# Performance work log

Measured on AMD Instinct MI355X. Metric: run time of the kernel, lower is better.

## Reference

```python
import jax, jax.numpy as jnp
import numpy as np

EPS = 1e-5

def _ln(x, g, b):
    m = jnp.mean(x, axis=-1, keepdims=True)
    v = jnp.mean(jnp.square(x - m), axis=-1, keepdims=True)
    return (x - m) * jax.lax.rsqrt(v + EPS) * g + b

def setup_inputs() -> dict:
    key = jax.random.key(0)
    ks = jax.random.split(key, 20)
    B, F = 262144, 768
    sizes = [F, 512, 256, 128, 1]  # LN(d_in) -> Linear(d_in, d_out) per block
    inp = {"input": jax.random.normal(ks[0], (B, F), dtype=jnp.float32)}
    for i in range(4):
        din, dout = sizes[i], sizes[i + 1]
        inp[f"g{i}"] = jnp.ones((din,), dtype=jnp.float32)
        inp[f"b{i}"] = jnp.zeros((din,), dtype=jnp.float32)
        bound = 1.0 / np.sqrt(din)
        inp[f"W{i}"] = jax.random.uniform(ks[1 + 2 * i], (dout, din), dtype=jnp.float32, minval=-bound, maxval=bound)
        inp[f"c{i}"] = jax.random.uniform(ks[2 + 2 * i], (dout,), dtype=jnp.float32, minval=-bound, maxval=bound)
    return inp

def reference(input, g0, b0, W0, c0, g1, b1, W1, c1, g2, b2, W2, c2, g3, b3, W3, c3):
    x = input
    params = [(g0, b0, W0, c0), (g1, b1, W1, c1), (g2, b2, W2, c2), (g3, b3, W3, c3)]
    for i, (g, b, W, c) in enumerate(params):
        x = _ln(x, g, b)
        x = x @ W.T + c
        if i != 3:
            x = jax.nn.elu(x)
    return jnp.squeeze(x, axis=-1)  # [B]
```

## Files before the change

kernel.cpp:

```cpp
#include <hip/hip_runtime.h>
#include <hip/hip_fp16.h>
#include <math.h>

typedef _Float16 half_t;
typedef half_t half2_t __attribute__((ext_vector_type(2)));
typedef half_t half4_t __attribute__((ext_vector_type(4)));
typedef half_t half8_t __attribute__((ext_vector_type(8)));
typedef float f32x4 __attribute__((ext_vector_type(4)));

#define LN_EPS 1e-5f
#define FDOT2(a, b, c) __builtin_amdgcn_fdot2((a), (b), (c), false)

__global__ void pack_weights(const float* __restrict__ W0, const float* __restrict__ g0,
                             const float* __restrict__ W1, const float* __restrict__ g1,
                             const float* __restrict__ W2, const float* __restrict__ g2,
                             half_t* __restrict__ ws) {
    int sid = blockIdx.x * 256 + threadIdx.x;
    const float* W; const float* g; int K, T, off;
    if (sid < 49152)      { W = W0; g = g0; K = 768; T = 24; off = 0; }
    else if (sid < 65536) { W = W1; g = g1; K = 512; T = 16; off = 49152; sid -= 49152; }
    else if (sid < 69632) { W = W2; g = g2; K = 256; T = 8;  off = 65536; sid -= 65536; }
    else return;
    const int l   = sid & 63;
    const int t   = (sid >> 6) % T;
    const int cbg = (sid >> 6) / T;
    const int n   = (l & 15) + 16 * cbg;
    const int k0  = 32 * t + 8 * (l >> 4);
    const float* src = W + (size_t)n * K + k0;
    const float* gs  = g + k0;
    half8_t v;
    #pragma unroll
    for (int jq = 0; jq < 8; jq++) v[jq] = (half_t)(src[jq] * gs[jq]);
    *(half8_t*)(ws + (size_t)(off + sid) * 8) = v;
}

__global__ void fold_bias(const float* __restrict__ W0, const float* __restrict__ g0,
                          const float* __restrict__ b0, const float* __restrict__ c0,
                          const float* __restrict__ W1, const float* __restrict__ g1,
                          const float* __restrict__ b1, const float* __restrict__ c1,
                          const float* __restrict__ W2, const float* __restrict__ g2,
                          const float* __restrict__ b2, const float* __restrict__ c2,
                          const float* __restrict__ W3, const float* __restrict__ g3,
                          const float* __restrict__ b3, const float* __restrict__ c3,
                          float* __restrict__ f) {
    const int gw   = (blockIdx.x * 256 + threadIdx.x) >> 6;
    const int lane = threadIdx.x & 63;
    if (gw == 896) {
        float s = 0.f, cb_ = 0.f;
        for (int k = lane; k < 128; k += 64) {
            const float wg = W3[k] * g3[k];
            f[1792 + k] = wg;
            s += wg; cb_ += W3[k] * b3[k];
        }
        #pragma unroll
        for (int m = 1; m < 64; m <<= 1) { s += __shfl_xor(s, m); cb_ += __shfl_xor(cb_, m); }
        if (lane == 0) { f[1920] = s; f[1921] = cb_ + c3[0]; }
        return;
    }
    const float *W, *g, *b, *cc; int K, n; float *sf, *cf;
    if (gw < 512)      { W = W0; g = g0; b = b0; cc = c0; K = 768; n = gw;       sf = f;        cf = f + 512; }
    else if (gw < 768) { W = W1; g = g1; b = b1; cc = c1; K = 512; n = gw - 512; sf = f + 1024; cf = f + 1280; }
    else if (gw < 896) { W = W2; g = g2; b = b2; cc = c2; K = 256; n = gw - 768; sf = f + 1536; cf = f + 1664; }
    else return;
    const float* Wr = W + (size_t)n * K;
    float s = 0.f, cb_ = 0.f;
    for (int k = lane; k < K; k += 64) { const float wg = Wr[k] * g[k]; s += wg; cb_ += Wr[k] * b[k]; }
    #pragma unroll
    for (int m = 1; m < 64; m <<= 1) { s += __shfl_xor(s, m); cb_ += __shfl_xor(cb_, m); }
    if (lane == 0) { sf[n] = s; cf[n] = cb_ + cc[n]; }
}

__global__ __launch_bounds__(512, 4)
void fused_mlp(const float* __restrict__ x_in,
               const half_t* __restrict__ W0p, const half_t* __restrict__ W1p,
               const half_t* __restrict__ W2p, const float* __restrict__ f,
               float* __restrict__ out)
{
    __shared__ half_t frag[32768];
    __shared__ float row_m[64], row_rs[64];
    __shared__ float ps[2][64], pq[2][64];
    __shared__ half2_t w3h[64];

    const int tid  = threadIdx.x;
    const int lane = tid & 63;
    const int wv   = tid >> 6;
    const int grp  = lane >> 4;
    const int cl   = lane & 15;
    const int row  = tid >> 3;
    const int jj   = tid & 7;
    const int rbw  = row >> 4;
    const long r0  = (long)blockIdx.x * 64;
    const float* xrow = x_in + (r0 + row) * 768;

    const int rb_s = wv & 3;
    const int th_s = wv >> 2;

    const float* s0f = f;        const float* c0f = f + 512;
    const float* s1f = f + 1024; const float* c1f = f + 1280;
    const float* s2f = f + 1536; const float* c2f = f + 1664;

    const half2_t one2 = {(half_t)1.f, (half_t)1.f};

    if (tid < 64) {
        half2_t w; w[0] = (half_t)f[1792 + 2 * tid]; w[1] = (half_t)f[1793 + 2 * tid];
        w3h[tid] = w;
    }

    float s = 0.f, ss = 0.f;
    f32x4 vb[4];

    auto stage_load = [&](int c) {
        const float* xp = xrow + 128 * c + 4 * jj;
        #pragma unroll
        for (int i = 0; i < 4; i++)
            vb[i] = __builtin_nontemporal_load((const f32x4*)(xp + 32 * i));
    };
    auto stage_write = [&](int c) {
        half_t* fb = frag + 8192 * (c & 1);
        const int hg = jj >> 1, jo = 4 * (jj & 1);
        #pragma unroll
        for (int i = 0; i < 4; i++) {
            const f32x4 v = vb[i];
            half2_t h01; h01[0] = (half_t)v[0]; h01[1] = (half_t)v[1];
            half2_t h23; h23[0] = (half_t)v[2]; h23[1] = (half_t)v[3];
            s  = FDOT2(h01, one2, s);  s  = FDOT2(h23, one2, s);
            ss = FDOT2(h01, h01, ss);  ss = FDOT2(h23, h23, ss);
            half4_t hv; hv[0] = h01[0]; hv[1] = h01[1]; hv[2] = h23[0]; hv[3] = h23[1];
            *(half4_t*)(&fb[((i * 4 + rbw) * 64 + ((row & 15) + 16 * hg)) * 8 + jo]) = hv;
        }
    };

    f32x4 acc0[4][4];
    #pragma unroll
    for (int rb = 0; rb < 4; rb++)
        #pragma unroll
        for (int cb = 0; cb < 4; cb++) acc0[rb][cb] = 0.f;

    auto gemm0 = [&](int c) {
        const half_t* fb = frag + 8192 * (c & 1);
        const half_t* wp = W0p + (size_t)(4 * wv * 24 + 4 * c) * 512 + lane * 8;
        half8_t bA[4], bB[4];
        #pragma unroll
        for (int cb = 0; cb < 4; cb++) bA[cb] = *(const half8_t*)(wp + cb * 12288);
        #pragma unroll
        for (int tt = 0; tt < 4; tt++) {
            half8_t* cur = (tt & 1) ? bB : bA;
            half8_t* nxt = (tt & 1) ? bA : bB;
            if (tt < 3) {
                #pragma unroll
                for (int cb = 0; cb < 4; cb++)
                    nxt[cb] = *(const half8_t*)(wp + (tt + 1) * 512 + cb * 12288);
            }
            half8_t af[4];
            #pragma unroll
            for (int rb = 0; rb < 4; rb++)
                af[rb] = *(const half8_t*)(&fb[((tt * 4 + rb) * 64 + lane) * 8]);
            #pragma unroll
            for (int cb = 0; cb < 4; cb++)
                #pragma unroll
                for (int rb = 0; rb < 4; rb++)
                    acc0[rb][cb] = __builtin_amdgcn_mfma_f32_16x16x32_f16(af[rb], cur[cb], acc0[rb][cb], 0, 0, 0);
        }
    };

    stage_load(0); stage_write(0);
    __syncthreads();
    #pragma unroll 1
    for (int c = 0; c < 6; c++) {
        if (c < 5) stage_load(c + 1);
        gemm0(c);
        if (c < 5) stage_write(c + 1);
        if (c == 4) {
            s  += __shfl_xor(s, 1);  s  += __shfl_xor(s, 2);  s  += __shfl_xor(s, 4);
            ss += __shfl_xor(ss, 1); ss += __shfl_xor(ss, 2); ss += __shfl_xor(ss, 4);
            if (jj == 0) {
                const float mm = s * (1.f / 768.f);
                row_m[row]  = mm;
                row_rs[row] = 1.f / sqrtf(ss * (1.f / 768.f) - mm * mm + LN_EPS);
            }
        }
        __syncthreads();
    }

    {
        float sv[4], cv[4];
        #pragma unroll
        for (int cb = 0; cb < 4; cb++) {
            const int c = cl + 16 * (4 * wv + cb);
            sv[cb] = s0f[c]; cv[cb] = c0f[c];
        }
        #pragma unroll
        for (int rb = 0; rb < 4; rb++)
            #pragma unroll
            for (int v = 0; v < 4; v++) {
                const int r = 16 * rb + 4 * grp + v;
                const float rm = row_m[r], rr = row_rs[r];
                #pragma unroll
                for (int cb = 0; cb < 4; cb++) {
                    float y = rr * (acc0[rb][cb][v] - rm * sv[cb]) + cv[cb];
                    acc0[rb][cb][v] = y > 0.f ? y : (__expf(y) - 1.f);
                }
            }
        #pragma unroll
        for (int cb = 0; cb < 4; cb++) {
            const int c = cl + 16 * (4 * wv + cb);
            const int t = c >> 5, j = c & 7, sc = 16 * ((c >> 3) & 3);
            #pragma unroll
            for (int rb = 0; rb < 4; rb++)
                #pragma unroll
                for (int v = 0; v < 4; v++)
                    frag[((t * 4 + rb) * 64 + (4 * grp + v + sc)) * 8 + j] = (half_t)acc0[rb][cb][v];
        }
    }
    __syncthreads();

    {
        float s_ = 0.f, q_ = 0.f;
        #pragma unroll
        for (int i = 0; i < 8; i++) {
            const int t = 8 * th_s + i;
            const half8_t h = *(const half8_t*)(&frag[((t * 4 + rb_s) * 64 + lane) * 8]);
            half2_t p0 = {h[0], h[1]}, p1 = {h[2], h[3]}, p2 = {h[4], h[5]}, p3 = {h[6], h[7]};
            s_ = FDOT2(p0, one2, s_); s_ = FDOT2(p1, one2, s_);
            s_ = FDOT2(p2, one2, s_); s_ = FDOT2(p3, one2, s_);
            q_ = FDOT2(p0, p0, q_);   q_ = FDOT2(p1, p1, q_);
            q_ = FDOT2(p2, p2, q_);   q_ = FDOT2(p3, p3, q_);
        }
        s_ += __shfl_xor(s_, 16); s_ += __shfl_xor(s_, 32);
        q_ += __shfl_xor(q_, 16); q_ += __shfl_xor(q_, 32);
        if (lane < 16) { ps[th_s][16 * rb_s + lane] = s_; pq[th_s][16 * rb_s + lane] = q_; }
    }
    __syncthreads();
    if (tid < 64) {
        const float a_ = ps[0][tid] + ps[1][tid];
        const float b_ = pq[0][tid] + pq[1][tid];
        const float mm = a_ * (1.f / 512.f);
        row_m[tid]  = mm;
        row_rs[tid] = 1.f / sqrtf(b_ * (1.f / 512.f) - mm * mm + LN_EPS);
    }

    f32x4 acc1[4][2];
    #pragma unroll
    for (int rb = 0; rb < 4; rb++) { acc1[rb][0] = 0.f; acc1[rb][1] = 0.f; }
    {
        const half_t* wp = W1p + (size_t)(2 * wv * 16) * 512 + lane * 8;
        half8_t bA[2], bB[2];
        bA[0] = *(const half8_t*)(wp);
        bA[1] = *(const half8_t*)(wp + 8192);
        #pragma unroll
        for (int t = 0; t < 16; t++) {
            half8_t* cur = (t & 1) ? bB : bA;
            half8_t* nxt = (t & 1) ? bA : bB;
            if (t < 15) {
                nxt[0] = *(const half8_t*)(wp + (t + 1) * 512);
                nxt[1] = *(const half8_t*)(wp + (t + 1) * 512 + 8192);
            }
            half8_t af[4];
            #pragma unroll
            for (int rb = 0; rb < 4; rb++)
                af[rb] = *(const half8_t*)(&frag[((t * 4 + rb) * 64 + lane) * 8]);
            #pragma unroll
            for (int cb = 0; cb < 2; cb++)
                #pragma unroll
                for (int rb = 0; rb < 4; rb++)
                    acc1[rb][cb] = __builtin_amdgcn_mfma_f32_16x16x32_f16(af[rb], cur[cb], acc1[rb][cb], 0, 0, 0);
        }
    }
    __syncthreads();

    {
        float sv[2], cv[2];
        #pragma unroll
        for (int cb = 0; cb < 2; cb++) {
            const int c = cl + 16 * (2 * wv + cb);
            sv[cb] = s1f[c]; cv[cb] = c1f[c];
        }
        #pragma unroll
        for (int rb = 0; rb < 4; rb++)
            #pragma unroll
            for (int v = 0; v < 4; v++) {
                const int r = 16 * rb + 4 * grp + v;
                const float rm = row_m[r], rr = row_rs[r];
                #pragma unroll
                for (int cb = 0; cb < 2; cb++) {
                    float y = rr * (acc1[rb][cb][v] - rm * sv[cb]) + cv[cb];
                    acc1[rb][cb][v] = y > 0.f ? y : (__expf(y) - 1.f);
                }
            }
        #pragma unroll
        for (int cb = 0; cb < 2; cb++) {
            const int c = cl + 16 * (2 * wv + cb);
            const int t = c >> 5, j = c & 7, sc = 16 * ((c >> 3) & 3);
            #pragma unroll
            for (int rb = 0; rb < 4; rb++)
                #pragma unroll
                for (int v = 0; v < 4; v++)
                    frag[((t * 4 + rb) * 64 + (4 * grp + v + sc)) * 8 + j] = (half_t)acc1[rb][cb][v];
        }
    }
    __syncthreads();

    {
        float s_ = 0.f, q_ = 0.f;
        #pragma unroll
        for (int i = 0; i < 4; i++) {
            const int t = 4 * th_s + i;
            const half8_t h = *(const half8_t*)(&frag[((t * 4 + rb_s) * 64 + lane) * 8]);
            half2_t p0 = {h[0], h[1]}, p1 = {h[2], h[3]}, p2 = {h[4], h[5]}, p3 = {h[6], h[7]};
            s_ = FDOT2(p0, one2, s_); s_ = FDOT2(p1, one2, s_);
            s_ = FDOT2(p2, one2, s_); s_ = FDOT2(p3, one2, s_);
            q_ = FDOT2(p0, p0, q_);   q_ = FDOT2(p1, p1, q_);
            q_ = FDOT2(p2, p2, q_);   q_ = FDOT2(p3, p3, q_);
        }
        s_ += __shfl_xor(s_, 16); s_ += __shfl_xor(s_, 32);
        q_ += __shfl_xor(q_, 16); q_ += __shfl_xor(q_, 32);
        if (lane < 16) { ps[th_s][16 * rb_s + lane] = s_; pq[th_s][16 * rb_s + lane] = q_; }
    }
    __syncthreads();
    if (tid < 64) {
        const float a_ = ps[0][tid] + ps[1][tid];
        const float b_ = pq[0][tid] + pq[1][tid];
        const float mm = a_ * (1.f / 256.f);
        row_m[tid]  = mm;
        row_rs[tid] = 1.f / sqrtf(b_ * (1.f / 256.f) - mm * mm + LN_EPS);
    }

    f32x4 acc2[4];
    #pragma unroll
    for (int rb = 0; rb < 4; rb++) acc2[rb] = 0.f;
    {
        const half_t* wp = W2p + (size_t)(wv * 8) * 512 + lane * 8;
        half8_t bA = *(const half8_t*)(wp);
        #pragma unroll
        for (int t = 0; t < 8; t++) {
            const half8_t cur = bA;
            if (t < 7) bA = *(const half8_t*)(wp + (t + 1) * 512);
            half8_t af[4];
            #pragma unroll
            for (int rb = 0; rb < 4; rb++)
                af[rb] = *(const half8_t*)(&frag[((t * 4 + rb) * 64 + lane) * 8]);
            #pragma unroll
            for (int rb = 0; rb < 4; rb++)
                acc2[rb] = __builtin_amdgcn_mfma_f32_16x16x32_f16(af[rb], cur, acc2[rb], 0, 0, 0);
        }
    }
    __syncthreads();

    {
        const int c2i = cl + 16 * wv;
        const float sv = s2f[c2i], cv = c2f[c2i];
        #pragma unroll
        for (int rb = 0; rb < 4; rb++)
            #pragma unroll
            for (int v = 0; v < 4; v++) {
                const int r = 16 * rb + 4 * grp + v;
                const float rm = row_m[r], rr = row_rs[r];
                float y = rr * (acc2[rb][v] - rm * sv) + cv;
                y = y > 0.f ? y : (__expf(y) - 1.f);
                frag[r * 136 + c2i] = (half_t)y;
            }
    }
    __syncthreads();

    {
        float s_ = 0.f, q_ = 0.f, d_ = 0.f;
        #pragma unroll
        for (int u = 0; u < 2; u++) {
            const int cb = jj * 16 + 8 * u;
            const int wi = cb >> 1;
            const half8_t h = *(const half8_t*)(frag + row * 136 + cb);
            half2_t p0 = {h[0], h[1]}, p1 = {h[2], h[3]}, p2 = {h[4], h[5]}, p3 = {h[6], h[7]};
            s_ = FDOT2(p0, one2, s_); s_ = FDOT2(p1, one2, s_);
            s_ = FDOT2(p2, one2, s_); s_ = FDOT2(p3, one2, s_);
            q_ = FDOT2(p0, p0, q_);   q_ = FDOT2(p1, p1, q_);
            q_ = FDOT2(p2, p2, q_);   q_ = FDOT2(p3, p3, q_);
            d_ = FDOT2(p0, w3h[wi], d_);     d_ = FDOT2(p1, w3h[wi + 1], d_);
            d_ = FDOT2(p2, w3h[wi + 2], d_); d_ = FDOT2(p3, w3h[wi + 3], d_);
        }
        s_ += __shfl_xor(s_, 1); s_ += __shfl_xor(s_, 2); s_ += __shfl_xor(s_, 4);
        q_ += __shfl_xor(q_, 1); q_ += __shfl_xor(q_, 2); q_ += __shfl_xor(q_, 4);
        d_ += __shfl_xor(d_, 1); d_ += __shfl_xor(d_, 2); d_ += __shfl_xor(d_, 4);
        if (jj == 0) {
            const float mm = s_ * (1.f / 128.f);
            const float rs = 1.f / sqrtf(q_ * (1.f / 128.f) - mm * mm + LN_EPS);
            out[r0 + row] = rs * (d_ - mm * f[1920]) + f[1921];
        }
    }
}

extern "C" void kernel_launch(void* const* d_in, const int* in_sizes, int n_in,
                              void* d_out, int out_size, void* d_ws, size_t ws_size,
                              hipStream_t stream) {
    const float* x  = (const float*)d_in[0];
    const float* g0 = (const float*)d_in[1];
    const float* b0 = (const float*)d_in[2];
    const float* W0 = (const float*)d_in[3];
    const float* c0 = (const float*)d_in[4];
    const float* g1 = (const float*)d_in[5];
    const float* b1 = (const float*)d_in[6];
    const float* W1 = (const float*)d_in[7];
    const float* c1 = (const float*)d_in[8];
    const float* g2 = (const float*)d_in[9];
    const float* b2 = (const float*)d_in[10];
    const float* W2 = (const float*)d_in[11];
    const float* c2 = (const float*)d_in[12];
    const float* g3 = (const float*)d_in[13];
    const float* b3 = (const float*)d_in[14];
    const float* W3 = (const float*)d_in[15];
    const float* c3 = (const float*)d_in[16];

    half_t* ws = (half_t*)d_ws;
    float*  f  = (float*)(ws + 557056);

    pack_weights<<<272, 256, 0, stream>>>(W0, g0, W1, g1, W2, g2, ws);
    fold_bias<<<225, 256, 0, stream>>>(W0, g0, b0, c0, W1, g1, b1, c1,
                                       W2, g2, b2, c2, W3, g3, b3, c3, f);

    const int nrows = in_sizes[0] / 768;
    fused_mlp<<<nrows / 64, 512, 0, stream>>>(
        x, ws, ws + 393216, ws + 524288, f, (float*)d_out);
}
```

Baseline: 545.5 us.

## Persistent kernel overlapping next tile's layer-0 GEMM with current tile's tail layers

Changes the kernel into a persistent grid of 256 blocks. Each block walks a range of 64-row tiles in a software pipeline: the input staging and layer-0 GEMM for tile i run interleaved with the LN/GEMM stages for layers 1-3 of tile i-1, using a double-buffered activation buffer. The aim is to hide global-memory streaming of the input behind the MFMA work of the later layers and to remove per-block launch and prologue cost. In exchange it needs much more LDS and more accumulator registers (launch bounds drop to 2 blocks per CU), assumes the tile count divides evenly by 256, and leaves W0 loads without explicit prefetch.

```diff
diff --git a/kernel.cpp b/kernel.cpp
--- a/kernel.cpp
+++ b/kernel.cpp
@@ -70,14 +70,16 @@
     if (lane == 0) { sf[n] = s; cf[n] = cb_ + cc[n]; }
 }
 
-__global__ __launch_bounds__(512, 4)
+__global__ __launch_bounds__(512, 2)
 void fused_mlp(const float* __restrict__ x_in,
                const half_t* __restrict__ W0p, const half_t* __restrict__ W1p,
                const half_t* __restrict__ W2p, const float* __restrict__ f,
-               float* __restrict__ out)
+               float* __restrict__ out, int ntiles)
 {
-    __shared__ half_t frag[32768];
+    __shared__ half_t x1buf[2][32768];
+    __shared__ half_t stg[2][6144];
     __shared__ float row_m[64], row_rs[64];
+    __shared__ float row_m0[64], row_rs0[64];
     __shared__ float ps[2][64], pq[2][64];
     __shared__ half2_t w3h[64];
 
@@ -89,16 +91,13 @@
     const int row  = tid >> 3;
     const int jj   = tid & 7;
     const int rbw  = row >> 4;
-    const long r0  = (long)blockIdx.x * 64;
-    const float* xrow = x_in + (r0 + row) * 768;
-
     const int rb_s = wv & 3;
     const int th_s = wv >> 2;
+    const long tile0 = (long)blockIdx.x * ntiles;
 
     const float* s0f = f;        const float* c0f = f + 512;
     const float* s1f = f + 1024; const float* c1f = f + 1280;
     const float* s2f = f + 1536; const float* c2f = f + 1664;
-
     const half2_t one2 = {(half_t)1.f, (half_t)1.f};
 
     if (tid < 64) {
@@ -107,284 +106,282 @@
     }
 
     float s = 0.f, ss = 0.f;
-    f32x4 vb[4];
-
-    auto stage_load = [&](int c) {
-        const float* xp = xrow + 128 * c + 4 * jj;
-        #pragma unroll
-        for (int i = 0; i < 4; i++)
-            vb[i] = __builtin_nontemporal_load((const f32x4*)(xp + 32 * i));
-    };
-    auto stage_write = [&](int c) {
-        half_t* fb = frag + 8192 * (c & 1);
-        const int hg = jj >> 1, jo = 4 * (jj & 1);
-        #pragma unroll
-        for (int i = 0; i < 4; i++) {
-            const f32x4 v = vb[i];
-            half2_t h01; h01[0] = (half_t)v[0]; h01[1] = (half_t)v[1];
-            half2_t h23; h23[0] = (half_t)v[2]; h23[1] = (half_t)v[3];
-            s  = FDOT2(h01, one2, s);  s  = FDOT2(h23, one2, s);
-            ss = FDOT2(h01, h01, ss);  ss = FDOT2(h23, h23, ss);
-            half4_t hv; hv[0] = h01[0]; hv[1] = h01[1]; hv[2] = h23[0]; hv[3] = h23[1];
-            *(half4_t*)(&fb[((i * 4 + rbw) * 64 + ((row & 15) + 16 * hg)) * 8 + jo]) = hv;
-        }
-    };
-
+    f32x4 vb[3];
     f32x4 acc0[4][4];
+    f32x4 acc1[4][2];
+    f32x4 acc2[4];
     #pragma unroll
     for (int rb = 0; rb < 4; rb++)
         #pragma unroll
         for (int cb = 0; cb < 4; cb++) acc0[rb][cb] = 0.f;
 
-    auto gemm0 = [&](int c) {
-        const half_t* fb = frag + 8192 * (c & 1);
-        const half_t* wp = W0p + (size_t)(4 * wv * 24 + 4 * c) * 512 + lane * 8;
-        half8_t bA[4], bB[4];
+    const float* xrow_base = x_in + (size_t)row * 768;
+
+    #pragma unroll 1
+    for (int i = 0; i <= ntiles; i++) {
+        const bool hasS = (i < ntiles);
+        const bool hasT = (i > 0);
+        const float* xrow = xrow_base + (size_t)(tile0 + i) * 49152;
+        half_t* xT = x1buf[(i + 1) & 1];
+
+        auto stage_load = [&](int c) {
+            const float* xp = xrow + 96 * c + 4 * jj;
+            #pragma unroll
+            for (int u = 0; u < 3; u++)
+                vb[u] = __builtin_nontemporal_load((const f32x4*)(xp + 32 * u));
+        };
+        auto stage_write = [&](int c) {
+            half_t* fb = stg[c & 1];
+            const int hg = jj >> 1, jo = 4 * (jj & 1);
+            #pragma unroll
+            for (int u = 0; u < 3; u++) {
+                const f32x4 v = vb[u];
+                half2_t h01; h01[0] = (half_t)v[0]; h01[1] = (half_t)v[1];
+                half2_t h23; h23[0] = (half_t)v[2]; h23[1] = (half_t)v[3];
+                s  = FDOT2(h01, one2, s);  s  = FDOT2(h23, one2, s);
+                ss = FDOT2(h01, h01, ss);  ss = FDOT2(h23, h23, ss);
+                half4_t hv; hv[0] = h01[0]; hv[1] = h01[1]; hv[2] = h23[0]; hv[3] = h23[1];
+                *(half4_t*)(&fb[((u * 4 + rbw) * 64 + ((row & 15) + 16 * hg)) * 8 + jo]) = hv;
+            }
+        };
+        auto gemm0c = [&](int c) {
+            const half_t* fb = stg[c & 1];
+            const half_t* wp = W0p + (size_t)(4 * wv * 24 + 3 * c) * 512 + lane * 8;
+            #pragma unroll
+            for (int tt = 0; tt < 3; tt++) {
+                half8_t af[4];
+                #pragma unroll
+                for (int rb = 0; rb < 4; rb++)
+                    af[rb] = *(const half8_t*)(&fb[((tt * 4 + rb) * 64 + lane) * 8]);
+                #pragma unroll
+                for (int cb = 0; cb < 4; cb++) {
+                    const half8_t bf = *(const half8_t*)(wp + tt * 512 + (size_t)cb * 12288);
+                    #pragma unroll
+                    for (int rb = 0; rb < 4; rb++)
+                        acc0[rb][cb] = __builtin_amdgcn_mfma_f32_16x16x32_f16(af[rb], bf, acc0[rb][cb], 0, 0, 0);
+                }
+            }
+        };
+
+        if (hasS) stage_load(0);
+        if (hasT) {
+            #pragma unroll
+            for (int cb = 0; cb < 4; cb++) {
+                const int c = cl + 16 * (4 * wv + cb);
+                const float sv = s0f[c], cv = c0f[c];
+                const int t = c >> 5, j = c & 7, sc = 16 * ((c >> 3) & 3);
+                #pragma unroll
+                for (int rb = 0; rb < 4; rb++)
+                    #pragma unroll
+                    for (int v = 0; v < 4; v++) {
+                        const int r = 16 * rb + 4 * grp + v;
+                        float y = row_rs0[r] * (acc0[rb][cb][v] - row_m0[r] * sv) + cv;
+                        y = y > 0.f ? y : (__expf(y) - 1.f);
+                        xT[((t * 4 + rb) * 64 + (4 * grp + v + sc)) * 8 + j] = (half_t)y;
+                    }
+            }
+        }
         #pragma unroll
-        for (int cb = 0; cb < 4; cb++) bA[cb] = *(const half8_t*)(wp + cb * 12288);
-        #pragma unroll
-        for (int tt = 0; tt < 4; tt++) {
-            half8_t* cur = (tt & 1) ? bB : bA;
-            half8_t* nxt = (tt & 1) ? bA : bB;
-            if (tt < 3) {
-                #pragma unroll
-                for (int cb = 0; cb < 4; cb++)
-                    nxt[cb] = *(const half8_t*)(wp + (tt + 1) * 512 + cb * 12288);
-            }
-            half8_t af[4];
+        for (int rb = 0; rb < 4; rb++)
+            #pragma unroll
+            for (int cb = 0; cb < 4; cb++) acc0[rb][cb] = 0.f;
+        if (hasS) stage_write(0);
+        __syncthreads();
+
+        if (hasS) stage_load(1);
+        if (hasT) {
+            float s_ = 0.f, q_ = 0.f;
+            #pragma unroll
+            for (int u = 0; u < 8; u++) {
+                const int t = 8 * th_s + u;
+                const half8_t h = *(const half8_t*)(&xT[((t * 4 + rb_s) * 64 + lane) * 8]);
+                half2_t p0 = {h[0], h[1]}, p1 = {h[2], h[3]}, p2 = {h[4], h[5]}, p3 = {h[6], h[7]};
+                s_ = FDOT2(p0, one2, s_); s_ = FDOT2(p1, one2, s_);
+                s_ = FDOT2(p2, one2, s_); s_ = FDOT2(p3, one2, s_);
+                q_ = FDOT2(p0, p0, q_);   q_ = FDOT2(p1, p1, q_);
+                q_ = FDOT2(p2, p2, q_);   q_ = FDOT2(p3, p3, q_);
+            }
+            s_ += __shfl_xor(s_, 16); s_ += __shfl_xor(s_, 32);
+            q_ += __shfl_xor(q_, 16); q_ += __shfl_xor(q_, 32);
+            if (lane < 16) { ps[th_s][16 * rb_s + lane] = s_; pq[th_s][16 * rb_s + lane] = q_; }
+        }
+        if (hasS) { gemm0c(0); stage_write(1); }
+        __syncthreads();
+
+        if (hasS) stage_load(2);
+        if (hasT) {
+            if (tid < 64) {
+                const float a_ = ps[0][tid] + ps[1][tid];
+                const float b_ = pq[0][tid] + pq[1][tid];
+                const float mm = a_ * (1.f / 512.f);
+                row_m[tid]  = mm;
+                row_rs[tid] = 1.f / sqrtf(b_ * (1.f / 512.f) - mm * mm + LN_EPS);
+            }
+            #pragma unroll
+            for (int rb = 0; rb < 4; rb++) { acc1[rb][0] = 0.f; acc1[rb][1] = 0.f; }
+            const half_t* wp = W1p + (size_t)(2 * wv * 16) * 512 + lane * 8;
+            #pragma unroll
+            for (int t = 0; t < 8; t++) {
+                half8_t af[4];
+                #pragma unroll
+                for (int rb = 0; rb < 4; rb++)
+                    af[rb] = *(const half8_t*)(&xT[((t * 4 + rb) * 64 + lane) * 8]);
+                #pragma unroll
+                for (int cb = 0; cb < 2; cb++) {
+                    const half8_t bf = *(const half8_t*)(wp + t * 512 + cb * 8192);
+                    #pragma unroll
+                    for (int rb = 0; rb < 4; rb++)
+                        acc1[rb][cb] = __builtin_amdgcn_mfma_f32_16x16x32_f16(af[rb], bf, acc1[rb][cb], 0, 0, 0);
+                }
+            }
+        }
+        if (hasS) { gemm0c(1); stage_write(2); }
+        __syncthreads();
+
+        if (hasS) stage_load(3);
+        if (hasT) {
+            const half_t* wp = W1p + (size_t)(2 * wv * 16) * 512 + lane * 8;
+            #pragma unroll
+            for (int t = 8; t < 16; t++) {
+                half8_t af[4];
+                #pragma unroll
+                for (int rb = 0; rb < 4; rb++)
+                    af[rb] = *(const half8_t*)(&xT[((t * 4 + rb) * 64 + lane) * 8]);
+                #pragma unroll
+                for (int cb = 0; cb < 2; cb++) {
+                    const half8_t bf = *(const half8_t*)(wp + t * 512 + cb * 8192);
+                    #pragma unroll
+                    for (int rb = 0; rb < 4; rb++)
+                        acc1[rb][cb] = __builtin_amdgcn_mfma_f32_16x16x32_f16(af[rb], bf, acc1[rb][cb], 0, 0, 0);
+                }
+            }
+        }
+        if (hasS) { gemm0c(2); stage_write(3); }
+        __syncthreads();
+
+        if (hasS) stage_load(4);
+        if (hasT) {
+            #pragma unroll
+            for (int cb = 0; cb < 2; cb++) {
+                const int c = cl + 16 * (2 * wv + cb);
+                const float sv = s1f[c], cv = c1f[c];
+                const int t = c >> 5, j = c & 7, sc = 16 * ((c >> 3) & 3);
+                #pragma unroll
+                for (int rb = 0; rb < 4; rb++)
+                    #pragma unroll
+                    for (int v = 0; v < 4; v++) {
+                        const int r = 16 * rb + 4 * grp + v;
+                        float y = row_rs[r] * (acc1[rb][cb][v] - row_m[r] * sv) + cv;
+                        y = y > 0.f ? y : (__expf(y) - 1.f);
+                        xT[((t * 4 + rb) * 64 + (4 * grp + v + sc)) * 8 + j] = (half_t)y;
+                    }
+            }
+        }
+        if (hasS) { gemm0c(3); stage_write(4); }
+        __syncthreads();
+
+        if (hasS) stage_load(5);
+        if (hasT) {
+            float s_ = 0.f, q_ = 0.f;
+            #pragma unroll
+            for (int u = 0; u < 4; u++) {
+                const int t = 4 * th_s + u;
+                const half8_t h = *(const half8_t*)(&xT[((t * 4 + rb_s) * 64 + lane) * 8]);
+                half2_t p0 = {h[0], h[1]}, p1 = {h[2], h[3]}, p2 = {h[4], h[5]}, p3 = {h[6], h[7]};
+                s_ = FDOT2(p0, one2, s_); s_ = FDOT2(p1, one2, s_);
+                s_ = FDOT2(p2, one2, s_); s_ = FDOT2(p3, one2, s_);
+                q_ = FDOT2(p0, p0, q_);   q_ = FDOT2(p1, p1, q_);
+                q_ = FDOT2(p2, p2, q_);   q_ = FDOT2(p3, p3, q_);
+            }
+            s_ += __shfl_xor(s_, 16); s_ += __shfl_xor(s_, 32);
+            q_ += __shfl_xor(q_, 16); q_ += __shfl_xor(q_, 32);
+            if (lane < 16) { ps[th_s][16 * rb_s + lane] = s_; pq[th_s][16 * rb_s + lane] = q_; }
+        }
+        if (hasS) { gemm0c(4); stage_write(5); }
+        __syncthreads();
+
+        if (hasS) stage_load(6);
+        if (hasT) {
+            if (tid < 64) {
+                const float a_ = ps[0][tid] + ps[1][tid];
+                const float b_ = pq[0][tid] + pq[1][tid];
+                const float mm = a_ * (1.f / 256.f);
+                row_m[tid]  = mm;
+                row_rs[tid] = 1.f / sqrtf(b_ * (1.f / 256.f) - mm * mm + LN_EPS);
+            }
+            #pragma unroll
+            for (int rb = 0; rb < 4; rb++) acc2[rb] = 0.f;
+            const half_t* wp = W2p + (size_t)(wv * 8) * 512 + lane * 8;
+            #pragma unroll
+            for (int t = 0; t < 8; t++) {
+                half8_t af[4];
+                #pragma unroll
+                for (int rb = 0; rb < 4; rb++)
+                    af[rb] = *(const half8_t*)(&xT[((t * 4 + rb) * 64 + lane) * 8]);
+                const half8_t bf = *(const half8_t*)(wp + t * 512);
+                #pragma unroll
+                for (int rb = 0; rb < 4; rb++)
+                    acc2[rb] = __builtin_amdgcn_mfma_f32_16x16x32_f16(af[rb], bf, acc2[rb], 0, 0, 0);
+            }
+        }
+        if (hasS) { gemm0c(5); stage_write(6); }
+        __syncthreads();
+
+        if (hasS) stage_load(7);
+        if (hasT) {
+            const int c2i = cl + 16 * wv;
+            const float sv = s2f[c2i], cv = c2f[c2i];
+            half_t* y3 = xT + 16384;
             #pragma unroll
             for (int rb = 0; rb < 4; rb++)
-                af[rb] = *(const half8_t*)(&fb[((tt * 4 + rb) * 64 + lane) * 8]);
-            #pragma unroll
-            for (int cb = 0; cb < 4; cb++)
-                #pragma unroll
-                for (int rb = 0; rb < 4; rb++)
-                    acc0[rb][cb] = __builtin_amdgcn_mfma_f32_16x16x32_f16(af[rb], cur[cb], acc0[rb][cb], 0, 0, 0);
-        }
-    };
-
-    stage_load(0); stage_write(0);
-    __syncthreads();
-    #pragma unroll 1
-    for (int c = 0; c < 6; c++) {
-        if (c < 5) stage_load(c + 1);
-        gemm0(c);
-        if (c < 5) stage_write(c + 1);
-        if (c == 4) {
+                #pragma unroll
+                for (int v = 0; v < 4; v++) {
+                    const int r = 16 * rb + 4 * grp + v;
+                    float y = row_rs[r] * (acc2[rb][v] - row_m[r] * sv) + cv;
+                    y = y > 0.f ? y : (__expf(y) - 1.f);
+                    y3[r * 136 + c2i] = (half_t)y;
+                }
+        }
+        if (hasS) { gemm0c(6); stage_write(7); }
+        __syncthreads();
+
+        if (hasT) {
+            const half_t* y3 = xT + 16384;
+            float s_ = 0.f, q_ = 0.f, d_ = 0.f;
+            #pragma unroll
+            for (int u = 0; u < 2; u++) {
+                const int cb = jj * 16 + 8 * u;
+                const int wi = cb >> 1;
+                const half8_t h = *(const half8_t*)(y3 + row * 136 + cb);
+                half2_t p0 = {h[0], h[1]}, p1 = {h[2], h[3]}, p2 = {h[4], h[5]}, p3 = {h[6], h[7]};
+                s_ = FDOT2(p0, one2, s_); s_ = FDOT2(p1, one2, s_);
+                s_ = FDOT2(p2, one2, s_); s_ = FDOT2(p3, one2, s_);
+                q_ = FDOT2(p0, p0, q_);   q_ = FDOT2(p1, p1, q_);
+                q_ = FDOT2(p2, p2, q_);   q_ = FDOT2(p3, p3, q_);
+                d_ = FDOT2(p0, w3h[wi], d_);     d_ = FDOT2(p1, w3h[wi + 1], d_);
+                d_ = FDOT2(p2, w3h[wi + 2], d_); d_ = FDOT2(p3, w3h[wi + 3], d_);
+            }
+            s_ += __shfl_xor(s_, 1); s_ += __shfl_xor(s_, 2); s_ += __shfl_xor(s_, 4);
+            q_ += __shfl_xor(q_, 1); q_ += __shfl_xor(q_, 2); q_ += __shfl_xor(q_, 4);
+            d_ += __shfl_xor(d_, 1); d_ += __shfl_xor(d_, 2); d_ += __shfl_xor(d_, 4);
+            if (jj == 0) {
+                const float mm = s_ * (1.f / 128.f);
+                const float rs = 1.f / sqrtf(q_ * (1.f / 128.f) - mm * mm + LN_EPS);
+                out[(tile0 + i - 1) * 64 + row] = rs * (d_ - mm * f[1920]) + f[1921];
+            }
+        }
+        if (hasS) {
+            gemm0c(7);
             s  += __shfl_xor(s, 1);  s  += __shfl_xor(s, 2);  s  += __shfl_xor(s, 4);
             ss += __shfl_xor(ss, 1); ss += __shfl_xor(ss, 2); ss += __shfl_xor(ss, 4);
             if (jj == 0) {
                 const float mm = s * (1.f / 768.f);
-                row_m[row]  = mm;
-                row_rs[row] = 1.f / sqrtf(ss * (1.f / 768.f) - mm * mm + LN_EPS);
-            }
-        }
-        __syncthreads();
-    }
-
-    {
-        float sv[4], cv[4];
-        #pragma unroll
-        for (int cb = 0; cb < 4; cb++) {
-            const int c = cl + 16 * (4 * wv + cb);
-            sv[cb] = s0f[c]; cv[cb] = c0f[c];
-        }
-        #pragma unroll
-        for (int rb = 0; rb < 4; rb++)
-            #pragma unroll
-            for (int v = 0; v < 4; v++) {
-                const int r = 16 * rb + 4 * grp + v;
-                const float rm = row_m[r], rr = row_rs[r];
-                #pragma unroll
-                for (int cb = 0; cb < 4; cb++) {
-                    float y = rr * (acc0[rb][cb][v] - rm * sv[cb]) + cv[cb];
-                    acc0[rb][cb][v] = y > 0.f ? y : (__expf(y) - 1.f);
-                }
-            }
-        #pragma unroll
-        for (int cb = 0; cb < 4; cb++) {
-            const int c = cl + 16 * (4 * wv + cb);
-            const int t = c >> 5, j = c & 7, sc = 16 * ((c >> 3) & 3);
-            #pragma unroll
-            for (int rb = 0; rb < 4; rb++)
-                #pragma unroll
-                for (int v = 0; v < 4; v++)
-                    frag[((t * 4 + rb) * 64 + (4 * grp + v + sc)) * 8 + j] = (half_t)acc0[rb][cb][v];
-        }
-    }
-    __syncthreads();
-
-    {
-        float s_ = 0.f, q_ = 0.f;
-        #pragma unroll
-        for (int i = 0; i < 8; i++) {
-            const int t = 8 * th_s + i;
-            const half8_t h = *(const half8_t*)(&frag[((t * 4 + rb_s) * 64 + lane) * 8]);
-            half2_t p0 = {h[0], h[1]}, p1 = {h[2], h[3]}, p2 = {h[4], h[5]}, p3 = {h[6], h[7]};
-            s_ = FDOT2(p0, one2, s_); s_ = FDOT2(p1, one2, s_);
-            s_ = FDOT2(p2, one2, s_); s_ = FDOT2(p3, one2, s_);
-            q_ = FDOT2(p0, p0, q_);   q_ = FDOT2(p1, p1, q_);
-            q_ = FDOT2(p2, p2, q_);   q_ = FDOT2(p3, p3, q_);
-        }
-        s_ += __shfl_xor(s_, 16); s_ += __shfl_xor(s_, 32);
-        q_ += __shfl_xor(q_, 16); q_ += __shfl_xor(q_, 32);
-        if (lane < 16) { ps[th_s][16 * rb_s + lane] = s_; pq[th_s][16 * rb_s + lane] = q_; }
-    }
-    __syncthreads();
-    if (tid < 64) {
-        const float a_ = ps[0][tid] + ps[1][tid];
-        const float b_ = pq[0][tid] + pq[1][tid];
-        const float mm = a_ * (1.f / 512.f);
-        row_m[tid]  = mm;
-        row_rs[tid] = 1.f / sqrtf(b_ * (1.f / 512.f) - mm * mm + LN_EPS);
-    }
-
-    f32x4 acc1[4][2];
-    #pragma unroll
-    for (int rb = 0; rb < 4; rb++) { acc1[rb][0] = 0.f; acc1[rb][1] = 0.f; }
-    {
-        const half_t* wp = W1p + (size_t)(2 * wv * 16) * 512 + lane * 8;
-        half8_t bA[2], bB[2];
-        bA[0] = *(const half8_t*)(wp);
-        bA[1] = *(const half8_t*)(wp + 8192);
-        #pragma unroll
-        for (int t = 0; t < 16; t++) {
-            half8_t* cur = (t & 1) ? bB : bA;
-            half8_t* nxt = (t & 1) ? bA : bB;
-            if (t < 15) {
-                nxt[0] = *(const half8_t*)(wp + (t + 1) * 512);
-                nxt[1] = *(const half8_t*)(wp + (t + 1) * 512 + 8192);
-            }
-            half8_t af[4];
-            #pragma unroll
-            for (int rb = 0; rb < 4; rb++)
-                af[rb] = *(const half8_t*)(&frag[((t * 4 + rb) * 64 + lane) * 8]);
-            #pragma unroll
-            for (int cb = 0; cb < 2; cb++)
-                #pragma unroll
-                for (int rb = 0; rb < 4; rb++)
-                    acc1[rb][cb] = __builtin_amdgcn_mfma_f32_16x16x32_f16(af[rb], cur[cb], acc1[rb][cb], 0, 0, 0);
-        }
-    }
-    __syncthreads();
-
-    {
-        float sv[2], cv[2];
-        #pragma unroll
-        for (int cb = 0; cb < 2; cb++) {
-            const int c = cl + 16 * (2 * wv + cb);
-            sv[cb] = s1f[c]; cv[cb] = c1f[c];
-        }
-        #pragma unroll
-        for (int rb = 0; rb < 4; rb++)
-            #pragma unroll
-            for (int v = 0; v < 4; v++) {
-                const int r = 16 * rb + 4 * grp + v;
-                const float rm = row_m[r], rr = row_rs[r];
-                #pragma unroll
-                for (int cb = 0; cb < 2; cb++) {
-                    float y = rr * (acc1[rb][cb][v] - rm * sv[cb]) + cv[cb];
-                    acc1[rb][cb][v] = y > 0.f ? y : (__expf(y) - 1.f);
-                }
-            }
-        #pragma unroll
-        for (int cb = 0; cb < 2; cb++) {
-            const int c = cl + 16 * (2 * wv + cb);
-            const int t = c >> 5, j = c & 7, sc = 16 * ((c >> 3) & 3);
-            #pragma unroll
-            for (int rb = 0; rb < 4; rb++)
-                #pragma unroll
-                for (int v = 0; v < 4; v++)
-                    frag[((t * 4 + rb) * 64 + (4 * grp + v + sc)) * 8 + j] = (half_t)acc1[rb][cb][v];
-        }
-    }
-    __syncthreads();
-
-    {
-        float s_ = 0.f, q_ = 0.f;
-        #pragma unroll
-        for (int i = 0; i < 4; i++) {
-            const int t = 4 * th_s + i;
-            const half8_t h = *(const half8_t*)(&frag[((t * 4 + rb_s) * 64 + lane) * 8]);
-            half2_t p0 = {h[0], h[1]}, p1 = {h[2], h[3]}, p2 = {h[4], h[5]}, p3 = {h[6], h[7]};
-            s_ = FDOT2(p0, one2, s_); s_ = FDOT2(p1, one2, s_);
-            s_ = FDOT2(p2, one2, s_); s_ = FDOT2(p3, one2, s_);
-            q_ = FDOT2(p0, p0, q_);   q_ = FDOT2(p1, p1, q_);
-            q_ = FDOT2(p2, p2, q_);   q_ = FDOT2(p3, p3, q_);
-        }
-        s_ += __shfl_xor(s_, 16); s_ += __shfl_xor(s_, 32);
-        q_ += __shfl_xor(q_, 16); q_ += __shfl_xor(q_, 32);
-        if (lane < 16) { ps[th_s][16 * rb_s + lane] = s_; pq[th_s][16 * rb_s + lane] = q_; }
-    }
-    __syncthreads();
-    if (tid < 64) {
-        const float a_ = ps[0][tid] + ps[1][tid];
-        const float b_ = pq[0][tid] + pq[1][tid];
-        const float mm = a_ * (1.f / 256.f);
-        row_m[tid]  = mm;
-        row_rs[tid] = 1.f / sqrtf(b_ * (1.f / 256.f) - mm * mm + LN_EPS);
-    }
-
-    f32x4 acc2[4];
-    #pragma unroll
-    for (int rb = 0; rb < 4; rb++) acc2[rb] = 0.f;
-    {
-        const half_t* wp = W2p + (size_t)(wv * 8) * 512 + lane * 8;
-        half8_t bA = *(const half8_t*)(wp);
-        #pragma unroll
-        for (int t = 0; t < 8; t++) {
-            const half8_t cur = bA;
-            if (t < 7) bA = *(const half8_t*)(wp + (t + 1) * 512);
-            half8_t af[4];
-            #pragma unroll
-            for (int rb = 0; rb < 4; rb++)
-                af[rb] = *(const half8_t*)(&frag[((t * 4 + rb) * 64 + lane) * 8]);
-            #pragma unroll
-            for (int rb = 0; rb < 4; rb++)
-                acc2[rb] = __builtin_amdgcn_mfma_f32_16x16x32_f16(af[rb], cur, acc2[rb], 0, 0, 0);
-        }
-    }
-    __syncthreads();
-
-    {
-        const int c2i = cl + 16 * wv;
-        const float sv = s2f[c2i], cv = c2f[c2i];
-        #pragma unroll
-        for (int rb = 0; rb < 4; rb++)
-            #pragma unroll
-            for (int v = 0; v < 4; v++) {
-                const int r = 16 * rb + 4 * grp + v;
-                const float rm = row_m[r], rr = row_rs[r];
-                float y = rr * (acc2[rb][v] - rm * sv) + cv;
-                y = y > 0.f ? y : (__expf(y) - 1.f);
-                frag[r * 136 + c2i] = (half_t)y;
-            }
-    }
-    __syncthreads();
-
-    {
-        float s_ = 0.f, q_ = 0.f, d_ = 0.f;
-        #pragma unroll
-        for (int u = 0; u < 2; u++) {
-            const int cb = jj * 16 + 8 * u;
-            const int wi = cb >> 1;
-            const half8_t h = *(const half8_t*)(frag + row * 136 + cb);
-            half2_t p0 = {h[0], h[1]}, p1 = {h[2], h[3]}, p2 = {h[4], h[5]}, p3 = {h[6], h[7]};
-            s_ = FDOT2(p0, one2, s_); s_ = FDOT2(p1, one2, s_);
-            s_ = FDOT2(p2, one2, s_); s_ = FDOT2(p3, one2, s_);
-            q_ = FDOT2(p0, p0, q_);   q_ = FDOT2(p1, p1, q_);
-            q_ = FDOT2(p2, p2, q_);   q_ = FDOT2(p3, p3, q_);
-            d_ = FDOT2(p0, w3h[wi], d_);     d_ = FDOT2(p1, w3h[wi + 1], d_);
-            d_ = FDOT2(p2, w3h[wi + 2], d_); d_ = FDOT2(p3, w3h[wi + 3], d_);
-        }
-        s_ += __shfl_xor(s_, 1); s_ += __shfl_xor(s_, 2); s_ += __shfl_xor(s_, 4);
-        q_ += __shfl_xor(q_, 1); q_ += __shfl_xor(q_, 2); q_ += __shfl_xor(q_, 4);
-        d_ += __shfl_xor(d_, 1); d_ += __shfl_xor(d_, 2); d_ += __shfl_xor(d_, 4);
-        if (jj == 0) {
-            const float mm = s_ * (1.f / 128.f);
-            const float rs = 1.f / sqrtf(q_ * (1.f / 128.f) - mm * mm + LN_EPS);
-            out[r0 + row] = rs * (d_ - mm * f[1920]) + f[1921];
-        }
+                row_m0[row]  = mm;
+                row_rs0[row] = 1.f / sqrtf(ss * (1.f / 768.f) - mm * mm + LN_EPS);
+            }
+            s = 0.f; ss = 0.f;
+        }
+        __syncthreads();
     }
 }
 
@@ -416,7 +413,8 @@
     fold_bias<<<225, 256, 0, stream>>>(W0, g0, b0, c0, W1, g1, b1, c1,
                                        W2, g2, b2, c2, W3, g3, b3, c3, f);
 
-    const int nrows = in_sizes[0] / 768;
-    fused_mlp<<<nrows / 64, 512, 0, stream>>>(
-        x, ws, ws + 393216, ws + 524288, f, (float*)d_out);
+    const int nrows  = in_sizes[0] / 768;
+    const int ntiles = (nrows / 64) / 256;
+    fused_mlp<<<256, 512, 0, stream>>>(
+        x, ws, ws + 393216, ws + 524288, f, (float*)d_out, ntiles);
 }
```

Result: slower. 1.011 ms (+85.3%).
